# Kernel optimization log

Measured on AMD Instinct MI355X. Metric: run time of the kernel, lower is better.

The kernel has to match this reference:

```python
import jax, jax.numpy as jnp
import numpy as np

META_HIDDEN = 32


def _meta_apply(t, mw1, mb1, mw2, mb2):
    # t: [..., 3] triples; meta MLP 3 -> META_HIDDEN -> 1 (ReLU)
    h = jax.nn.relu(jnp.einsum('...k,hk->...h', t, mw1) + mb1)
    return jnp.einsum('...h,h->...', h, mw2[0]) + mb2[0]


def _meta_update_layer(v_in, w, v_out, mw1, mb1, mw2, mb2):
    # v_in: [I] (batch-0 input activations), w: [O, I], v_out: [O] (batch-0 output activations)
    # Builds the triples [v_i, w_ij, v_j] for every (i, j) pair and runs one batched meta pass.
    t = jnp.stack([
        jnp.broadcast_to(v_in[None, :], w.shape),
        w,
        jnp.broadcast_to(v_out[:, None], w.shape),
    ], axis=-1)  # [O, I, 3]
    return _meta_apply(t, mw1, mb1, mw2, mb2)  # [O, I] new weights


def setup_inputs() -> dict:
    key = jax.random.key(0)
    ks = jax.random.split(key, 12)
    I, H1, H2, O, B = 1024, 2048, 2048, 1024, 32
    def lin(kw, fan_in, fan_out):
        s = 1.0 / np.sqrt(fan_in)
        return jax.random.uniform(kw, (fan_out, fan_in), jnp.float32, -s, s)
    x = jax.random.normal(ks[0], (B, I), jnp.float32)
    w1 = lin(ks[1], I, H1); b1 = jax.random.uniform(ks[2], (H1,), jnp.float32, -1/np.sqrt(I), 1/np.sqrt(I))
    w2 = lin(ks[3], H1, H2); b2 = jax.random.uniform(ks[4], (H2,), jnp.float32, -1/np.sqrt(H1), 1/np.sqrt(H1))
    w3 = lin(ks[5], H2, O); b3 = jax.random.uniform(ks[6], (O,), jnp.float32, -1/np.sqrt(H2), 1/np.sqrt(H2))
    # meta network 3 -> META_HIDDEN -> 1
    mw1 = lin(ks[7], 3, META_HIDDEN); mb1 = jax.random.uniform(ks[8], (META_HIDDEN,), jnp.float32, -1/np.sqrt(3), 1/np.sqrt(3))
    mw2 = lin(ks[9], META_HIDDEN, 1); mb2 = jax.random.uniform(ks[10], (1,), jnp.float32, -1/np.sqrt(META_HIDDEN), 1/np.sqrt(META_HIDDEN))
    return {"x": x, "w1": w1, "b1": b1, "w2": w2, "b2": b2, "w3": w3, "b3": b3,
            "mw1": mw1, "mb1": mb1, "mw2": mw2, "mb2": mb2}


def reference(x, w1, b1, w2, b2, w3, b3, mw1, mb1, mw2, mb2):
    # Main 3-layer MLP forward (ReLU after every layer, including the last, as in the source).
    a0 = x
    a1 = jax.nn.relu(a0 @ w1.T + b1)
    a2 = jax.nn.relu(a1 @ w2.T + b2)
    out = jax.nn.relu(a2 @ w3.T + b3)
    # Per-weight meta update: original code loops over every (input, output) neuron pair of
    # each fc weight and writes meta_weight([v_i, w_ij, v_j]) back into the weight.
    # Only batch row 0 of the activations is used (impulse[i].data[0, idx]).
    nw1 = _meta_update_layer(a0[0], w1, a1[0], mw1, mb1, mw2, mb2)
    nw2 = _meta_update_layer(a1[0], w2, a2[0], mw1, mb1, mw2, mb2)
    nw3 = _meta_update_layer(a2[0], w3, out[0], mw1, mb1, mw2, mb2)
    return out, nw1, nw2, nw3
```

## Files before the change

kernel.cpp:

```cpp
#include <hip/hip_runtime.h>

#define NT 256

typedef unsigned int uint;
typedef unsigned short ushort_t;
typedef float f2 __attribute__((ext_vector_type(2)));
typedef short bh8 __attribute__((ext_vector_type(8)));
typedef float f32x4 __attribute__((ext_vector_type(4)));
typedef uint u32x4 __attribute__((ext_vector_type(4)));

__device__ __forceinline__ void gload16(const float* g, float* l) {
  __builtin_amdgcn_global_load_lds(
      (const __attribute__((address_space(1))) void*)g,
      (__attribute__((address_space(3))) void*)l, 16, 0, 0);
}

__device__ __forceinline__ uint hi2(float a, float b) {
  return (__float_as_uint(a) >> 16) | (__float_as_uint(b) & 0xffff0000u);
}
__device__ __forceinline__ uint lo2(float a, float b) {
  const float r0 = a - __uint_as_float(__float_as_uint(a) & 0xffff0000u);
  const float r1 = b - __uint_as_float(__float_as_uint(b) & 0xffff0000u);
  return hi2(r0, r1);
}
__device__ __forceinline__ void split8v(float4 v0, float4 v1, bh8& hi, bh8& lo) {
  u32x4 h = {hi2(v0.x, v0.y), hi2(v0.z, v0.w), hi2(v1.x, v1.y), hi2(v1.z, v1.w)};
  u32x4 t = {lo2(v0.x, v0.y), lo2(v0.z, v0.w), lo2(v1.x, v1.y), lo2(v1.z, v1.w)};
  hi = __builtin_bit_cast(bh8, h);
  lo = __builtin_bit_cast(bh8, t);
}

__device__ __forceinline__ void meta_body(
    int g,
    const float* __restrict__ w1, const float* __restrict__ w2, const float* __restrict__ w3,
    const float* __restrict__ a0, const float* __restrict__ r1, const float* __restrict__ r2,
    const float* __restrict__ bb1, const float* __restrict__ bb2, const float* __restrict__ bb3,
    float* __restrict__ n1, float* __restrict__ n2, float* __restrict__ n3,
    const float* __restrict__ mw1, const float* __restrict__ mb1,
    const float* __restrict__ mw2, const float* __restrict__ mb2) {
  const int n1c = (2048 * 1024) / 8;
  const int n2c = (2048 * 2048) / 8;

  const float* W; const float* vin; const float* bias; float* nw;
  int sh, e;
  if (g < n1c)            { W = w1; vin = a0; bias = bb1; nw = n1; sh = 10; e = g; }
  else if (g < n1c + n2c) { W = w2; vin = r1; bias = bb2; nw = n2; sh = 11; e = g - n1c; }
  else                    { W = w3; vin = r2; bias = bb3; nw = n3; sh = 11; e = g - n1c - n2c; }

  const int base = e << 3;
  const int o = base >> sh;
  const int i0 = base & ((1 << sh) - 1);
  const int tid = threadIdx.x;

  f2 wv[4], vv[4];
  {
    float4 t0 = *reinterpret_cast<const float4*>(&W[base]);
    float4 t1 = *reinterpret_cast<const float4*>(&W[base + 4]);
    wv[0] = (f2){t0.x, t0.y}; wv[1] = (f2){t0.z, t0.w};
    wv[2] = (f2){t1.x, t1.y}; wv[3] = (f2){t1.z, t1.w};
    float4 u0 = *reinterpret_cast<const float4*>(&vin[i0]);
    float4 u1 = *reinterpret_cast<const float4*>(&vin[i0 + 4]);
    vv[0] = (f2){u0.x, u0.y}; vv[1] = (f2){u0.z, u0.w};
    vv[2] = (f2){u1.x, u1.y}; vv[3] = (f2){u1.z, u1.w};
  }

  float part = 0.f;
  #pragma unroll
  for (int p = 0; p < 4; ++p)
    part += wv[p].x * vv[p].x + wv[p].y * vv[p].y;
  #pragma unroll
  for (int m = 32; m >= 1; m >>= 1)
    part += __shfl_xor(part, m, 64);
  __shared__ float msum[4];
  if ((tid & 63) == 0) msum[tid >> 6] = part;
  __syncthreads();
  float vo;
  if (sh == 10) vo = (tid < 128) ? (msum[0] + msum[1]) : (msum[2] + msum[3]);
  else          vo = (msum[0] + msum[1]) + (msum[2] + msum[3]);
  vo = fmaxf(vo + bias[o], 0.f);

  const float c2 = mb2[0];
  float r[32];
  #pragma unroll
  for (int j = 0; j < 32; ++j)
    r[j] = fmaf(mw1[3 * j + 2], vo, mb1[j]);

  f2 acc[4];
  #pragma unroll
  for (int p = 0; p < 4; ++p) acc[p] = (f2){c2, c2};

  const f2 zero = (f2){0.f, 0.f};
  #pragma unroll
  for (int j = 0; j < 32; ++j) {
    const float aj = mw1[3 * j];
    const float bj = mw1[3 * j + 1];
    const float mj = mw2[j];
    const f2 a2v = (f2){aj, aj};
    const f2 b2v = (f2){bj, bj};
    const f2 m2v = (f2){mj, mj};
    const f2 r2v = (f2){r[j], r[j]};
    #pragma unroll
    for (int p = 0; p < 4; ++p) {
#if __has_builtin(__builtin_elementwise_fma) && __has_builtin(__builtin_elementwise_max)
      f2 q = __builtin_elementwise_fma(a2v, vv[p], r2v);
      f2 h = __builtin_elementwise_fma(b2v, wv[p], q);
      h = __builtin_elementwise_max(h, zero);
      acc[p] = __builtin_elementwise_fma(m2v, h, acc[p]);
#else
      f2 h;
      h.x = fmaxf(fmaf(bj, wv[p].x, fmaf(aj, vv[p].x, r[j])), 0.f);
      h.y = fmaxf(fmaf(bj, wv[p].y, fmaf(aj, vv[p].y, r[j])), 0.f);
      acc[p].x = fmaf(mj, h.x, acc[p].x);
      acc[p].y = fmaf(mj, h.y, acc[p].y);
#endif
    }
  }

  *reinterpret_cast<float4*>(&nw[base])     = make_float4(acc[0].x, acc[0].y, acc[1].x, acc[1].y);
  *reinterpret_cast<float4*>(&nw[base + 4]) = make_float4(acc[2].x, acc[2].y, acc[3].x, acc[3].y);
}

template<int KL, int OBL, int AF32>
__device__ __forceinline__ void gemm_fwd(
    int gb, int tid,
    const float* __restrict__ Af32, const ushort_t* __restrict__ Ahi,
    const ushort_t* __restrict__ Alo,
    const float* __restrict__ W, int K, int O,
    float* __restrict__ P, float* __restrict__ Wt) {
  const int ob = gb & ((1 << OBL) - 1);
  const int sl = gb >> OBL;
  const int w = tid >> 6, l = tid & 63;
  const int l15 = l & 15, lk = l >> 4;
  const int b0 = (w & 1) << 4;
  const int ow = (w >> 1) << 6;
  const int obase = ob << 7;
  const int kbeg = sl * KL;
  const int bA = b0 + l15;

  f32x4 acc[4];
  #pragma unroll
  for (int of = 0; of < 4; ++of)
    #pragma unroll
    for (int e = 0; e < 4; ++e) acc[of][e] = 0.f;

  #pragma unroll 1
  for (int c = 0; c < KL / 32; ++c) {
    const int kc = kbeg + (c << 5);
    bh8 ahi, alo;
    const int kk = kc + (lk << 3);
    if constexpr (AF32) {
      const float4 v0 = *reinterpret_cast<const float4*>(&Af32[(size_t)bA * K + kk]);
      const float4 v1 = *reinterpret_cast<const float4*>(&Af32[(size_t)bA * K + kk + 4]);
      split8v(v0, v1, ahi, alo);
    } else {
      ahi = *reinterpret_cast<const bh8*>(&Ahi[(size_t)bA * K + kk]);
      alo = *reinterpret_cast<const bh8*>(&Alo[(size_t)bA * K + kk]);
    }
    #pragma unroll
    for (int q = 0; q < 4; ++q) {
      const int s = (q << 8) + tid;
      const int r = s >> 3;
      const int p = s & 7;
      const float* gp = &W[(size_t)(obase + r) * K + kc + ((p ^ (r & 7)) << 2)];
      gload16(gp, Wt + ((s & ~63) << 2));
    }
    __syncthreads();

    #pragma unroll
    for (int of = 0; of < 4; ++of) {
      const int lr = ow + (of << 4) + l15;
      const int cb = lk << 1;
      const float4 w0 = *reinterpret_cast<const float4*>(
          &Wt[(lr << 5) + ((cb ^ (lr & 7)) << 2)]);
      const float4 w1 = *reinterpret_cast<const float4*>(
          &Wt[(lr << 5) + (((cb + 1) ^ (lr & 7)) << 2)]);
      bh8 whi, wlo;
      split8v(w0, w1, whi, wlo);
      acc[of] = __builtin_amdgcn_mfma_f32_16x16x32_bf16(ahi, whi, acc[of], 0, 0, 0);
      acc[of] = __builtin_amdgcn_mfma_f32_16x16x32_bf16(ahi, wlo, acc[of], 0, 0, 0);
      acc[of] = __builtin_amdgcn_mfma_f32_16x16x32_bf16(alo, whi, acc[of], 0, 0, 0);
    }
    __syncthreads();
  }

  #pragma unroll
  for (int of = 0; of < 4; ++of) {
    const int o = obase + ow + (of << 4) + l15;
    #pragma unroll
    for (int r = 0; r < 4; ++r) {
      const int b = b0 + lk * 4 + r;
      P[((size_t)sl * 32 + b) * O + o] = acc[of][r];
    }
  }
}

template<int MODE, int OSH>
__device__ __forceinline__ void red_body(
    int lbid, int tid, const float* __restrict__ P, const float* __restrict__ bias,
    ushort_t* __restrict__ aHi, ushort_t* __restrict__ aLo,
    float* __restrict__ outF, float* __restrict__ row0) {
  const int idx = lbid * NT + tid;
  const int b = idx >> OSH;
  const int o = idx & ((1 << OSH) - 1);
  float s = 0.f;
  #pragma unroll
  for (int sl = 0; sl < 16; ++sl)
    s += P[(size_t)((sl * 32 + b) << OSH) + o];
  const float v = fmaxf(s + bias[o], 0.f);
  if constexpr (MODE == 0) {
    const uint u = __float_as_uint(v);
    aHi[(size_t)(b << OSH) + o] = (ushort_t)(u >> 16);
    const float hi = __uint_as_float(u & 0xffff0000u);
    aLo[(size_t)(b << OSH) + o] = (ushort_t)(__float_as_uint(v - hi) >> 16);
  } else {
    outF[(size_t)(b << OSH) + o] = v;
  }
  if (row0 != nullptr && b == 0) row0[o] = v;
}

template<int KL, int OBL, int AF32, int RMODE, int ROSH>
__global__ __launch_bounds__(NT) void fused(
    int nGemm, const float* Af32, const ushort_t* Ahi, const ushort_t* Alo,
    const float* W, int K, int O, float* P,
    int nRed, const float* RP, const float* Rb, ushort_t* rHi, ushort_t* rLo,
    float* rOut, float* rRow0,
    int mStart,
    const float* w1, const float* w2, const float* w3,
    const float* a0, const float* r1, const float* r2,
    const float* bb1, const float* bb2, const float* bb3,
    float* n1, float* n2, float* n3,
    const float* mw1, const float* mb1, const float* mw2, const float* mb2) {
  const int bid = blockIdx.x;
  const int tid = threadIdx.x;
  if (bid < nGemm) {
    __shared__ float Wt[128 * 32];
    gemm_fwd<KL, OBL, AF32>(bid, tid, Af32, Ahi, Alo, W, K, O, P, Wt);
    return;
  }
  int b = bid - nGemm;
  if (b < nRed) { red_body<RMODE, ROSH>(b, tid, RP, Rb, rHi, rLo, rOut, rRow0); return; }
  b -= nRed;
  const int g = mStart + b * NT + tid;
  meta_body(g, w1, w2, w3, a0, r1, r2, bb1, bb2, bb3,
            n1, n2, n3, mw1, mb1, mw2, mb2);
}

extern "C" void kernel_launch(void* const* d_in, const int* in_sizes, int n_in,
                              void* d_out, int out_size, void* d_ws, size_t ws_size,
                              hipStream_t stream) {
  const float* x   = (const float*)d_in[0];
  const float* w1  = (const float*)d_in[1];
  const float* b1  = (const float*)d_in[2];
  const float* w2  = (const float*)d_in[3];
  const float* b2  = (const float*)d_in[4];
  const float* w3  = (const float*)d_in[5];
  const float* b3  = (const float*)d_in[6];
  const float* mw1 = (const float*)d_in[7];
  const float* mb1 = (const float*)d_in[8];
  const float* mw2 = (const float*)d_in[9];
  const float* mb2 = (const float*)d_in[10];

  float* out = (float*)d_out;
  float* n1  = out + 32 * 1024;
  float* n2  = n1 + 2048 * 1024;
  float* n3  = n2 + 2048 * 2048;

  float* ws = (float*)d_ws;
  float* row01  = ws;
  float* row02  = row01 + 2048;
  ushort_t* a1hi = (ushort_t*)(row02 + 2048);
  ushort_t* a1lo = a1hi + 65536;
  ushort_t* a2hi = a1lo + 65536;
  ushort_t* a2lo = a2hi + 65536;
  float* P1 = (float*)(a2lo + 65536);
  float* P2 = P1 + 1048576;
  float* P3 = P2 + 1048576;

  #define MARGS w1, w2, w3, x, row01, row02, b1, b2, b3, n1, n2, n3, mw1, mb1, mw2, mb2
  #define NOGEMM 0, (const float*)nullptr, (const ushort_t*)nullptr, (const ushort_t*)nullptr, (const float*)nullptr, 0, 0, (float*)nullptr
  #define NORED  0, (const float*)nullptr, (const float*)nullptr, (ushort_t*)nullptr, (ushort_t*)nullptr, (float*)nullptr, (float*)nullptr

  fused<64, 4, 1, 0, 11><<<1280, NT, 0, stream>>>(
      256, x, nullptr, nullptr, w1, 1024, 2048, P1,
      NORED, 0, MARGS);

  fused<64, 4, 0, 0, 11><<<256, NT, 0, stream>>>(
      NOGEMM,
      256, P1, b1, a1hi, a1lo, nullptr, row01,
      0, MARGS);

  fused<128, 4, 0, 0, 11><<<2304, NT, 0, stream>>>(
      256, nullptr, a1hi, a1lo, w2, 2048, 2048, P2,
      NORED, 262144, MARGS);

  fused<64, 4, 0, 0, 11><<<256, NT, 0, stream>>>(
      NOGEMM,
      256, P2, b2, a2hi, a2lo, nullptr, row02,
      0, MARGS);

  fused<128, 3, 0, 0, 11><<<1152, NT, 0, stream>>>(
      128, nullptr, a2hi, a2lo, w3, 2048, 1024, P3,
      NORED, 786432, MARGS);

  fused<64, 4, 0, 1, 10><<<128, NT, 0, stream>>>(
      NOGEMM,
      128, P3, b3, nullptr, nullptr, out, nullptr,
      0, MARGS);

  #undef MARGS
  #undef NOGEMM
  #undef NORED
}
```

Baseline: 52.30 us.

## Fuse split-K reduction into next GEMM's A load, add row-0 GEMV blocks

Drops the separate reduction kernels after layers 1 and 2. The next GEMM now sums the split-K partials, adds bias and applies ReLU while loading its A operand, and splits the result to bf16 hi/lo in registers. The batch-0 activation rows that the meta update needs are computed by extra GEMV blocks that run alongside the GEMM in the same launch. K-slices are doubled, which halves the partial buffers, and the launch count drops from six to four. In exchange, each GEMM block rereads 8 partial slices per A tile, the row-0 dot products are computed a second time, and there is less split-K parallelism.

After: 89.87 us. +71.8%, slower.

```diff
diff --git a/kernel.cpp b/kernel.cpp
--- a/kernel.cpp
+++ b/kernel.cpp
@@ -120,11 +120,39 @@
   *reinterpret_cast<float4*>(&nw[base + 4]) = make_float4(acc[2].x, acc[2].y, acc[3].x, acc[3].y);
 }
 
-template<int KL, int OBL, int AF32>
+__device__ __forceinline__ void gemv_body(
+    int lbid, int tid,
+    const float* __restrict__ vX, const float* __restrict__ vW,
+    const float* __restrict__ vB, float* __restrict__ vR, int vK) {
+  const int w = tid >> 6, l = tid & 63;
+  const int obase = lbid * 16 + w * 4;
+  const int nt = vK >> 8;
+  float4 xv[8];
+  #pragma unroll 8
+  for (int t = 0; t < nt; ++t)
+    xv[t] = *reinterpret_cast<const float4*>(&vX[(l + (t << 6)) << 2]);
+  #pragma unroll
+  for (int q = 0; q < 4; ++q) {
+    const int o = obase + q;
+    const float* wr = vW + (size_t)o * vK;
+    float a = 0.f;
+    #pragma unroll 8
+    for (int t = 0; t < nt; ++t) {
+      const float4 wv = *reinterpret_cast<const float4*>(&wr[(l + (t << 6)) << 2]);
+      a = fmaf(wv.x, xv[t].x, a); a = fmaf(wv.y, xv[t].y, a);
+      a = fmaf(wv.z, xv[t].z, a); a = fmaf(wv.w, xv[t].w, a);
+    }
+    #pragma unroll
+    for (int m = 32; m >= 1; m >>= 1)
+      a += __shfl_xor(a, m, 64);
+    if (l == 0) vR[o] = fmaxf(a + vB[o], 0.f);
+  }
+}
+
+template<int KL, int OBL, int AMODE>
 __device__ __forceinline__ void gemm_fwd(
     int gb, int tid,
-    const float* __restrict__ Af32, const ushort_t* __restrict__ Ahi,
-    const ushort_t* __restrict__ Alo,
+    const float* __restrict__ Asrc, const float* __restrict__ Abias,
     const float* __restrict__ W, int K, int O,
     float* __restrict__ P, float* __restrict__ Wt) {
   const int ob = gb & ((1 << OBL) - 1);
@@ -146,15 +174,28 @@
   #pragma unroll 1
   for (int c = 0; c < KL / 32; ++c) {
     const int kc = kbeg + (c << 5);
+    const int kk = kc + (lk << 3);
     bh8 ahi, alo;
-    const int kk = kc + (lk << 3);
-    if constexpr (AF32) {
-      const float4 v0 = *reinterpret_cast<const float4*>(&Af32[(size_t)bA * K + kk]);
-      const float4 v1 = *reinterpret_cast<const float4*>(&Af32[(size_t)bA * K + kk + 4]);
+    if constexpr (AMODE == 0) {
+      const float4 v0 = *reinterpret_cast<const float4*>(&Asrc[(size_t)bA * K + kk]);
+      const float4 v1 = *reinterpret_cast<const float4*>(&Asrc[(size_t)bA * K + kk + 4]);
       split8v(v0, v1, ahi, alo);
     } else {
-      ahi = *reinterpret_cast<const bh8*>(&Ahi[(size_t)bA * K + kk]);
-      alo = *reinterpret_cast<const bh8*>(&Alo[(size_t)bA * K + kk]);
+      float4 s0 = *reinterpret_cast<const float4*>(&Abias[kk]);
+      float4 s1 = *reinterpret_cast<const float4*>(&Abias[kk + 4]);
+      #pragma unroll
+      for (int q2 = 0; q2 < 8; ++q2) {
+        const float* pp = &Asrc[((size_t)(q2 * 32) + bA) * K + kk];
+        const float4 p0 = *reinterpret_cast<const float4*>(pp);
+        const float4 p1 = *reinterpret_cast<const float4*>(pp + 4);
+        s0.x += p0.x; s0.y += p0.y; s0.z += p0.z; s0.w += p0.w;
+        s1.x += p1.x; s1.y += p1.y; s1.z += p1.z; s1.w += p1.w;
+      }
+      s0.x = fmaxf(s0.x, 0.f); s0.y = fmaxf(s0.y, 0.f);
+      s0.z = fmaxf(s0.z, 0.f); s0.w = fmaxf(s0.w, 0.f);
+      s1.x = fmaxf(s1.x, 0.f); s1.y = fmaxf(s1.y, 0.f);
+      s1.z = fmaxf(s1.z, 0.f); s1.w = fmaxf(s1.w, 0.f);
+      split8v(s0, s1, ahi, alo);
     }
     #pragma unroll
     for (int q = 0; q < 4; ++q) {
@@ -194,36 +235,10 @@
   }
 }
 
-template<int MODE, int OSH>
-__device__ __forceinline__ void red_body(
-    int lbid, int tid, const float* __restrict__ P, const float* __restrict__ bias,
-    ushort_t* __restrict__ aHi, ushort_t* __restrict__ aLo,
-    float* __restrict__ outF, float* __restrict__ row0) {
-  const int idx = lbid * NT + tid;
-  const int b = idx >> OSH;
-  const int o = idx & ((1 << OSH) - 1);
-  float s = 0.f;
-  #pragma unroll
-  for (int sl = 0; sl < 16; ++sl)
-    s += P[(size_t)((sl * 32 + b) << OSH) + o];
-  const float v = fmaxf(s + bias[o], 0.f);
-  if constexpr (MODE == 0) {
-    const uint u = __float_as_uint(v);
-    aHi[(size_t)(b << OSH) + o] = (ushort_t)(u >> 16);
-    const float hi = __uint_as_float(u & 0xffff0000u);
-    aLo[(size_t)(b << OSH) + o] = (ushort_t)(__float_as_uint(v - hi) >> 16);
-  } else {
-    outF[(size_t)(b << OSH) + o] = v;
-  }
-  if (row0 != nullptr && b == 0) row0[o] = v;
-}
-
-template<int KL, int OBL, int AF32, int RMODE, int ROSH>
-__global__ __launch_bounds__(NT) void fused(
-    int nGemm, const float* Af32, const ushort_t* Ahi, const ushort_t* Alo,
-    const float* W, int K, int O, float* P,
-    int nRed, const float* RP, const float* Rb, ushort_t* rHi, ushort_t* rLo,
-    float* rOut, float* rRow0,
+template<int KL, int OBL, int AMODE>
+__global__ __launch_bounds__(NT) void fusedK(
+    int nGemm, const float* Asrc, const float* Abias, const float* W, int K, int O, float* P,
+    int nGemv, const float* vX, const float* vW, const float* vB, float* vR, int vK,
     int mStart,
     const float* w1, const float* w2, const float* w3,
     const float* a0, const float* r1, const float* r2,
@@ -234,15 +249,28 @@
   const int tid = threadIdx.x;
   if (bid < nGemm) {
     __shared__ float Wt[128 * 32];
-    gemm_fwd<KL, OBL, AF32>(bid, tid, Af32, Ahi, Alo, W, K, O, P, Wt);
+    gemm_fwd<KL, OBL, AMODE>(bid, tid, Asrc, Abias, W, K, O, P, Wt);
     return;
   }
   int b = bid - nGemm;
-  if (b < nRed) { red_body<RMODE, ROSH>(b, tid, RP, Rb, rHi, rLo, rOut, rRow0); return; }
-  b -= nRed;
-  const int g = mStart + b * NT + tid;
+  if (b < nGemv) { gemv_body(b, tid, vX, vW, vB, vR, vK); return; }
+  b -= nGemv;
+  const int g = (mStart + b) * NT + tid;
   meta_body(g, w1, w2, w3, a0, r1, r2, bb1, bb2, bb3,
             n1, n2, n3, mw1, mb1, mw2, mb2);
+}
+
+__global__ __launch_bounds__(NT) void red3k(
+    const float* __restrict__ P, const float* __restrict__ bias,
+    float* __restrict__ outF) {
+  const int idx = blockIdx.x * NT + threadIdx.x;
+  const int b = idx >> 10;
+  const int o = idx & 1023;
+  float s = 0.f;
+  #pragma unroll
+  for (int sl = 0; sl < 8; ++sl)
+    s += P[(size_t)((sl * 32 + b) << 10) + o];
+  outF[(size_t)(b << 10) + o] = fmaxf(s + bias[o], 0.f);
 }
 
 extern "C" void kernel_launch(void* const* d_in, const int* in_sizes, int n_in,
@@ -266,48 +294,30 @@
   float* n3  = n2 + 2048 * 2048;
 
   float* ws = (float*)d_ws;
-  float* row01  = ws;
-  float* row02  = row01 + 2048;
-  ushort_t* a1hi = (ushort_t*)(row02 + 2048);
-  ushort_t* a1lo = a1hi + 65536;
-  ushort_t* a2hi = a1lo + 65536;
-  ushort_t* a2lo = a2hi + 65536;
-  float* P1 = (float*)(a2lo + 65536);
-  float* P2 = P1 + 1048576;
-  float* P3 = P2 + 1048576;
+  float* row01 = ws;
+  float* row02 = row01 + 2048;
+  float* P1 = row02 + 2048;
+  float* P2 = P1 + 524288;
+  float* P3 = P2 + 524288;
 
   #define MARGS w1, w2, w3, x, row01, row02, b1, b2, b3, n1, n2, n3, mw1, mb1, mw2, mb2
-  #define NOGEMM 0, (const float*)nullptr, (const ushort_t*)nullptr, (const ushort_t*)nullptr, (const float*)nullptr, 0, 0, (float*)nullptr
-  #define NORED  0, (const float*)nullptr, (const float*)nullptr, (ushort_t*)nullptr, (ushort_t*)nullptr, (float*)nullptr, (float*)nullptr
-
-  fused<64, 4, 1, 0, 11><<<1280, NT, 0, stream>>>(
-      256, x, nullptr, nullptr, w1, 1024, 2048, P1,
-      NORED, 0, MARGS);
-
-  fused<64, 4, 0, 0, 11><<<256, NT, 0, stream>>>(
-      NOGEMM,
-      256, P1, b1, a1hi, a1lo, nullptr, row01,
+
+  fusedK<128, 4, 0><<<1280, NT, 0, stream>>>(
+      128, x, nullptr, w1, 1024, 2048, P1,
+      128, x, w1, b1, row01, 1024,
       0, MARGS);
 
-  fused<128, 4, 0, 0, 11><<<2304, NT, 0, stream>>>(
-      256, nullptr, a1hi, a1lo, w2, 2048, 2048, P2,
-      NORED, 262144, MARGS);
-
-  fused<64, 4, 0, 0, 11><<<256, NT, 0, stream>>>(
-      NOGEMM,
-      256, P2, b2, a2hi, a2lo, nullptr, row02,
-      0, MARGS);
-
-  fused<128, 3, 0, 0, 11><<<1152, NT, 0, stream>>>(
-      128, nullptr, a2hi, a2lo, w3, 2048, 1024, P3,
-      NORED, 786432, MARGS);
-
-  fused<64, 4, 0, 1, 10><<<128, NT, 0, stream>>>(
-      NOGEMM,
-      128, P3, b3, nullptr, nullptr, out, nullptr,
-      0, MARGS);
+  fusedK<256, 4, 1><<<2304, NT, 0, stream>>>(
+      128, P1, b1, w2, 2048, 2048, P2,
+      128, row01, w2, b2, row02, 2048,
+      1024, MARGS);
+
+  fusedK<256, 3, 1><<<1088, NT, 0, stream>>>(
+      64, P2, b2, w3, 2048, 1024, P3,
+      0, nullptr, nullptr, nullptr, nullptr, 0,
+      3072, MARGS);
+
+  red3k<<<128, NT, 0, stream>>>(P3, b3, out);
 
   #undef MARGS
-  #undef NOGEMM
-  #undef NORED
-}
+}
```
